# Kernel tuning notes

Measured on AMD Instinct MI355X. Metric: run time of the kernel, lower is better.

## Reference

```python
import jax, jax.numpy as jnp
import numpy as np


def setup_inputs() -> dict:
    key = jax.random.key(0)
    k1, k2, k3 = jax.random.split(key, 3)
    N, E, D_IN, D_OUT = 100000, 1600000, 64, 64
    x = jax.random.normal(k1, (N, D_IN), dtype=jnp.float32)
    edge_index = jax.random.randint(k2, (2, E), 0, N, dtype=jnp.int64)
    # Glorot-style init for the GCN weight, zero bias (PyG defaults)
    W = jax.random.normal(k3, (D_IN, D_OUT), dtype=jnp.float32) * (1.0 / np.sqrt(D_IN))
    b = jnp.zeros((D_OUT,), dtype=jnp.float32)
    return {"x": x, "edge_index": edge_index, "W": W, "b": b}


def reference(x, edge_index, W, b):
    # GCNConv (PyG semantics, add_self_loops=True, normalize=True) followed by
    # Dropout (eval mode -> identity) and ReLU.
    N = x.shape[0]
    # Linear transform first (small GEMM)
    xw = x @ W  # [N, D_OUT]
    # Add self-loops
    loops = jnp.arange(N, dtype=edge_index.dtype)
    row = jnp.concatenate([edge_index[0], loops])  # source nodes
    col = jnp.concatenate([edge_index[1], loops])  # destination nodes
    # Symmetric degree normalization: deg over destination index (PyG gcn_norm)
    ones = jnp.ones(col.shape[0], dtype=xw.dtype)
    deg = jax.ops.segment_sum(ones, col, num_segments=N)
    deg_inv_sqrt = jnp.where(deg > 0, jax.lax.rsqrt(deg), 0.0)
    norm = deg_inv_sqrt[row] * deg_inv_sqrt[col]  # [E+N]
    # Gather source features, scale, scatter-add to destinations
    msgs = norm[:, None] * xw[row]  # [E+N, D_OUT]
    out = jax.ops.segment_sum(msgs, col, num_segments=N)
    out = out + b
    # dropout in eval mode is identity
    return jax.nn.relu(out)
```

## Files before the change

kernel.cpp:

```cpp
#include <hip/hip_runtime.h>
#include <hip/hip_fp16.h>


#define D 64
#define BW 256
#define CAPB 4800
#define CAPL (CAPB + 3 * BW)
#define EPT 16
#define PART_T 512
#define EPB (PART_T * EPT)
#define NBMAX 512

typedef __attribute__((ext_vector_type(8))) short bf16x8;
typedef __attribute__((ext_vector_type(4))) float f32x4;

__device__ __forceinline__ unsigned short f2bf(float f) {
    unsigned u = __float_as_uint(f);
    u += 0x7FFFu + ((u >> 16) & 1u);
    return (unsigned short)(u >> 16);
}

__global__ __launch_bounds__(512)
void k_cnt(const int* __restrict__ col, int* __restrict__ cnts,
           unsigned short* __restrict__ WT, const float* __restrict__ W,
           unsigned short* __restrict__ xw_h, int E, int NBUCK, int N) {
    __shared__ int lh[NBMAX];
    int tid = threadIdx.x;
    for (int i = tid; i < NBUCK; i += 512) lh[i] = 0;
    __syncthreads();
    int e0 = blockIdx.x * EPB + tid;
#pragma unroll
    for (int i = 0; i < EPT; ++i) {
        int e = e0 + i * 512;
        if (e < E)
            atomicAdd(&lh[__builtin_nontemporal_load(col + e) >> 8], 1);
    }
    __syncthreads();
    size_t cb = (size_t)blockIdx.x * NBUCK;
    for (int j = tid; j < NBUCK; j += 512) cnts[cb + j] = lh[j];
    if (blockIdx.x == 0) {
        for (int i = tid; i < 4096; i += 512) {
            int n = i >> 6, k = i & 63;
            WT[i] = f2bf(W[k * 64 + n]);
        }
        if (tid < 32) ((unsigned*)xw_h)[(size_t)N * 32 + tid] = 0u;
    }
}

__global__ __launch_bounds__(256)
void k_scan(const int* __restrict__ cnts, int* __restrict__ bases,
            int* __restrict__ bsz, int NB1, int NBUCK) {
    __shared__ int wsum[4];
    int b = blockIdx.x, t = threadIdx.x, lane = t & 63, wv = t >> 6;
    int v = (t < NB1) ? cnts[(size_t)t * NBUCK + b] : 0;
    int inc = v;
#pragma unroll
    for (int o = 1; o < 64; o <<= 1) {
        int u = __shfl_up(inc, o);
        if (lane >= o) inc += u;
    }
    if (lane == 63) wsum[wv] = inc;
    __syncthreads();
    int woff = 0;
#pragma unroll
    for (int w = 0; w < 4; ++w) woff += (w < wv) ? wsum[w] : 0;
    if (t < NB1) bases[(size_t)t * NBUCK + b] = woff + inc - v;
    if (t == 255) bsz[b] = woff + inc;
}

__global__ __launch_bounds__(512, 4)
void k_part(const int* __restrict__ row, const int* __restrict__ col,
            const int* __restrict__ bases, int* __restrict__ dense,
            int E, int NBUCK) {
    __shared__ int lh[NBMAX];
    __shared__ int lst[NBMAX + 1];
    __shared__ int bas[NBMAX];
    __shared__ int wsc[8];
    __shared__ int srtv[EPB];
    int tid = threadIdx.x;
    size_t bb = (size_t)blockIdx.x * NBUCK;
    for (int i = tid; i < NBUCK; i += 512) {
        lh[i] = 0;
        bas[i] = bases[bb + i];
    }
    __syncthreads();
    int e0 = blockIdx.x * EPB + tid;
    int rr[EPT], cc[EPT], pp[EPT];
#pragma unroll
    for (int i = 0; i < EPT; ++i) {
        int e = e0 + i * 512;
        if (e < E) {
            cc[i] = __builtin_nontemporal_load(col + e);
            rr[i] = __builtin_nontemporal_load(row + e);
            pp[i] = atomicAdd(&lh[cc[i] >> 8], 1);
        } else {
            cc[i] = -1;
        }
    }
    __syncthreads();
    int lane = tid & 63, wv = tid >> 6;
    int v = (tid < NBUCK) ? lh[tid] : 0;
    int inc = v;
#pragma unroll
    for (int o = 1; o < 64; o <<= 1) {
        int u = __shfl_up(inc, o);
        if (lane >= o) inc += u;
    }
    if (lane == 63) wsc[wv] = inc;
    __syncthreads();
    int woff = 0;
#pragma unroll
    for (int w = 0; w < 8; ++w) woff += (w < wv) ? wsc[w] : 0;
    if (tid < NBUCK) lst[tid] = woff + inc - v;
    int tot = min(EPB, E - blockIdx.x * EPB);
    if (tid == 0) lst[NBUCK] = tot;
    __syncthreads();
#pragma unroll
    for (int i = 0; i < EPT; ++i) {
        if (cc[i] >= 0)
            srtv[lst[cc[i] >> 8] + pp[i]] = (rr[i] << 8) | (cc[i] & 255);
    }
    __syncthreads();
    for (int p = tid; p < tot; p += 512) {
        int lo = 0, hi = NBUCK;
        while (hi - lo > 1) {
            int mid = (lo + hi) >> 1;
            if (lst[mid] <= p) lo = mid; else hi = mid;
        }
        int gpos = bas[lo] + (p - lst[lo]);
        if (gpos < CAPB) dense[(size_t)lo * CAPB + gpos] = srtv[p];
    }
}

__global__ __launch_bounds__(256, 4)
void k_gemm(const float* __restrict__ x, const unsigned short* __restrict__ WT,
            const int* __restrict__ dense, const int* __restrict__ bsz,
            unsigned char* __restrict__ deg8, unsigned short* __restrict__ xw_h,
            int N, int NT) {
    __shared__ int lh[BW];
    int tid = threadIdx.x, b = blockIdx.x;
    lh[tid] = 0;
    __syncthreads();
    int tot = min(bsz[b], CAPB);
    const int* dn = dense + (size_t)b * CAPB;
    for (int i = tid; i < tot; i += 256)
        atomicAdd(&lh[__builtin_nontemporal_load(dn + i) & 255], 1);
    __syncthreads();
    {
        int node = b * BW + tid;
        if (node < N) deg8[node] = (unsigned char)min(lh[tid], 255);
    }
    int lane = tid & 63, wv = tid >> 6;
    int m = lane & 15, quad = lane >> 4;
    bf16x8 Bf[4][2];
#pragma unroll
    for (int t = 0; t < 4; ++t)
#pragma unroll
        for (int s = 0; s < 2; ++s)
            Bf[t][s] = *(const bf16x8*)(WT + (t * 16 + m) * 64 + s * 32 + quad * 8);
#pragma unroll
    for (int s = 0; s < 4; ++s) {
        int mt = b * 16 + s * 4 + wv;
        if (mt >= NT) continue;
        int row0 = mt * 16;
        const float* xr = x + (size_t)(row0 + m) * 64 + quad * 8;
        f32x4 a0 = __builtin_nontemporal_load((const f32x4*)(xr));
        f32x4 a1 = __builtin_nontemporal_load((const f32x4*)(xr + 4));
        f32x4 a2 = __builtin_nontemporal_load((const f32x4*)(xr + 32));
        f32x4 a3 = __builtin_nontemporal_load((const f32x4*)(xr + 36));
        bf16x8 A0, A1;
        A0[0] = (short)f2bf(a0[0]); A0[1] = (short)f2bf(a0[1]);
        A0[2] = (short)f2bf(a0[2]); A0[3] = (short)f2bf(a0[3]);
        A0[4] = (short)f2bf(a1[0]); A0[5] = (short)f2bf(a1[1]);
        A0[6] = (short)f2bf(a1[2]); A0[7] = (short)f2bf(a1[3]);
        A1[0] = (short)f2bf(a2[0]); A1[1] = (short)f2bf(a2[1]);
        A1[2] = (short)f2bf(a2[2]); A1[3] = (short)f2bf(a2[3]);
        A1[4] = (short)f2bf(a3[0]); A1[5] = (short)f2bf(a3[1]);
        A1[6] = (short)f2bf(a3[2]); A1[7] = (short)f2bf(a3[3]);
        f32x4 acc[4];
#pragma unroll
        for (int t = 0; t < 4; ++t) {
            acc[t] = (f32x4){0.f, 0.f, 0.f, 0.f};
            acc[t] = __builtin_amdgcn_mfma_f32_16x16x32_bf16(Bf[t][0], A0, acc[t], 0, 0, 0);
            acc[t] = __builtin_amdgcn_mfma_f32_16x16x32_bf16(Bf[t][1], A1, acc[t], 0, 0, 0);
        }
        float dsc = rsqrtf((float)(lh[(row0 + m) & 255] + 1));
        unsigned short* op = xw_h + (size_t)(row0 + m) * 64 + quad * 4;
#pragma unroll
        for (int t = 0; t < 4; ++t) {
            __half2 h0, h1;
            h0.x = __float2half(acc[t][0] * dsc); h0.y = __float2half(acc[t][1] * dsc);
            h1.x = __float2half(acc[t][2] * dsc); h1.y = __float2half(acc[t][3] * dsc);
            uint2 u; u.x = *(unsigned*)&h0; u.y = *(unsigned*)&h1;
            *(uint2*)(op + t * 16) = u;
        }
    }
}

__global__ __launch_bounds__(512, 4)
void k_gather(const int* __restrict__ dense, const int* __restrict__ bsz,
              const unsigned char* __restrict__ deg8,
              const uint2* __restrict__ xwh, const float* __restrict__ bias,
              float* __restrict__ out, int N) {
    __shared__ int lh[BW], stt[BW], cur[BW];
    __shared__ int wsum[4];
    __shared__ __align__(16) int srtL[CAPL];
    int b = blockIdx.x, tid = threadIdx.x, lane = tid & 63;
    int v = 0, vp = 0, inc = 0;
    if (tid < BW) {
        int node = b * BW + tid;
        v = (node < N) ? (int)deg8[node] : 0;
        lh[tid] = v;
        vp = (v + 3) & ~3; inc = vp;
#pragma unroll
        for (int o = 1; o < 64; o <<= 1) {
            int u = __shfl_up(inc, o);
            if (lane >= o) inc += u;
        }
        if (lane == 63) wsum[tid >> 6] = inc;
    }
    __syncthreads();
    if (tid < BW) {
        int wv4 = tid >> 6, woff = 0;
#pragma unroll
        for (int w = 0; w < 4; ++w) woff += (w < wv4) ? wsum[w] : 0;
        int st = woff + inc - vp;
        stt[tid] = st;
        cur[tid] = st;
    }
    __syncthreads();
    int tot = min(bsz[b], CAPB);
    const int* dn = dense + (size_t)b * CAPB;
    for (int i = tid; i < tot; i += 512) {
        int val = __builtin_nontemporal_load(dn + i);
        int pos = atomicAdd(&cur[val & 255], 1);
        if (pos < CAPL) srtL[pos] = val >> 8;
    }
    __syncthreads();
    if (tid < BW) {
        int e = stt[tid] + v, ep = min(stt[tid] + vp, CAPL);
        for (; e < ep; ++e) srtL[e] = N;
    }
    __syncthreads();
    int l = lane & 15;
    int ng = lane >> 4;
    int wv = tid >> 6;
    const float4 bb = ((const float4*)bias)[l];
#define ADDV(h)                                                     \
    {                                                               \
        __half2 h0 = *(__half2*)&(h).x, h1 = *(__half2*)&(h).y;     \
        float2 f0 = __half22float2(h0), f1 = __half22float2(h1);    \
        acc.x += f0.x; acc.y += f0.y; acc.z += f1.x; acc.w += f1.y; \
    }
    for (int g = 0; g < 8; ++g) {
        int nn = wv * 32 + g * 4 + ng;
        int node = b * BW + nn;
        bool active = node < N;
        float4 acc = make_float4(0.f, 0.f, 0.f, 0.f);
        int k = 0, s0 = 0;
        if (active) {
            k = lh[nn]; s0 = stt[nn];
            uint2 hs = xwh[(size_t)node * 16 + l];
            ADDV(hs);
        }
        int kp = (k + 3) & ~3;
        if (s0 + kp > CAPL) kp = (CAPL > s0) ? ((CAPL - s0) & ~3) : 0;
        if (kp > 0) {
            int4 rv = *(const int4*)&srtL[s0];
            int j = 0;
            while (true) {
                uint2 va = xwh[(size_t)rv.x * 16 + l];
                uint2 vb = xwh[(size_t)rv.y * 16 + l];
                uint2 vc = xwh[(size_t)rv.z * 16 + l];
                uint2 vd = xwh[(size_t)rv.w * 16 + l];
                j += 4;
                bool more = j < kp;
                if (more) rv = *(const int4*)&srtL[s0 + j];
                ADDV(va); ADDV(vb); ADDV(vc); ADDV(vd);
                if (!more) break;
            }
        }
        if (active) {
            float dn2 = rsqrtf((float)(k + 1));
            f32x4 o;
            o[0] = fmaxf(fmaf(dn2, acc.x, bb.x), 0.f);
            o[1] = fmaxf(fmaf(dn2, acc.y, bb.y), 0.f);
            o[2] = fmaxf(fmaf(dn2, acc.z, bb.z), 0.f);
            o[3] = fmaxf(fmaf(dn2, acc.w, bb.w), 0.f);
            __builtin_nontemporal_store(o, (f32x4*)(out + ((size_t)node * 16 + l) * 4));
        }
    }
#undef ADDV
}

extern "C" void kernel_launch(void* const* d_in, const int* in_sizes, int n_in,
                              void* d_out, int out_size, void* d_ws, size_t ws_size,
                              hipStream_t stream) {
    const float* x    = (const float*)d_in[0];
    const int*   ei   = (const int*)d_in[1];
    const float* W    = (const float*)d_in[2];
    const float* bias = (const float*)d_in[3];
    float* out = (float*)d_out;

    const int N = in_sizes[0] / D;
    const int E = in_sizes[1] / 2;
    const int* row = ei;
    const int* col = ei + E;

    const int NBUCK = (N + BW - 1) / BW;
    const int NB1   = (E + EPB - 1) / EPB;
    const int NT    = (N + 15) / 16;

    char* ws = (char*)d_ws;
    size_t o = 0;
    unsigned short* xw_h = (unsigned short*)(ws + o);
    o += (size_t)(N + 1) * D * sizeof(unsigned short);
    int* dense = (int*)(ws + o); o += (size_t)NBUCK * CAPB * sizeof(int);
    int* cnts  = (int*)(ws + o); o += (size_t)NB1 * NBUCK * sizeof(int);
    int* bases = (int*)(ws + o); o += (size_t)NB1 * NBUCK * sizeof(int);
    int* bsz   = (int*)(ws + o); o += (size_t)NBUCK * sizeof(int);
    o = (o + 15) & ~(size_t)15;
    unsigned char* deg8 = (unsigned char*)(ws + o); o += (size_t)N;
    o = (o + 15) & ~(size_t)15;
    unsigned short* WT = (unsigned short*)(ws + o); o += 4096 * sizeof(unsigned short);

    k_cnt <<<NB1,   512, 0, stream>>>(col, cnts, WT, W, xw_h, E, NBUCK, N);
    k_scan<<<NBUCK, 256, 0, stream>>>(cnts, bases, bsz, NB1, NBUCK);
    k_part<<<NB1,   512, 0, stream>>>(row, col, bases, dense, E, NBUCK);
    k_gemm<<<NBUCK, 256, 0, stream>>>(x, WT, dense, bsz, deg8, xw_h, N, NT);
    k_gather<<<NBUCK, 512, 0, stream>>>(dense, bsz, deg8, (const uint2*)xw_h,
                                        bias, out, N);
}
```

Measured before the change: 172.5 us.

## Replace count/scan passes with atomic bucket reservation and persistent half-bucket gather

Drops the separate counting and scan kernels. Each partition block now reserves its slice of every destination bucket with a global atomicAdd on padded counters, which a memset clears first. The gather kernel becomes a persistent grid of 512 blocks that pull half-bucket work items from an atomic ticket, using a smaller LDS list for more occupancy and a software-pipelined neighbour load loop. This removes one full pass over the edges and a kernel launch. In exchange, edge order within a bucket becomes nondeterministic, the gather filters every bucket entry twice, and a shrunken per-half capacity could truncate high-degree halves.

```diff
diff --git a/kernel.cpp b/kernel.cpp
--- a/kernel.cpp
+++ b/kernel.cpp
@@ -5,11 +5,12 @@
 #define D 64
 #define BW 256
 #define CAPB 4800
-#define CAPL (CAPB + 3 * BW)
+#define CAPL 2944
 #define EPT 16
 #define PART_T 512
 #define EPB (PART_T * EPT)
 #define NBMAX 512
+#define GSTRIDE 16
 
 typedef __attribute__((ext_vector_type(8))) short bf16x8;
 typedef __attribute__((ext_vector_type(4))) float f32x4;
@@ -21,74 +22,24 @@
 }
 
 __global__ __launch_bounds__(512)
-void k_cnt(const int* __restrict__ col, int* __restrict__ cnts,
-           unsigned short* __restrict__ WT, const float* __restrict__ W,
-           unsigned short* __restrict__ xw_h, int E, int NBUCK, int N) {
-    __shared__ int lh[NBMAX];
-    int tid = threadIdx.x;
-    for (int i = tid; i < NBUCK; i += 512) lh[i] = 0;
-    __syncthreads();
-    int e0 = blockIdx.x * EPB + tid;
-#pragma unroll
-    for (int i = 0; i < EPT; ++i) {
-        int e = e0 + i * 512;
-        if (e < E)
-            atomicAdd(&lh[__builtin_nontemporal_load(col + e) >> 8], 1);
-    }
-    __syncthreads();
-    size_t cb = (size_t)blockIdx.x * NBUCK;
-    for (int j = tid; j < NBUCK; j += 512) cnts[cb + j] = lh[j];
-    if (blockIdx.x == 0) {
-        for (int i = tid; i < 4096; i += 512) {
-            int n = i >> 6, k = i & 63;
-            WT[i] = f2bf(W[k * 64 + n]);
-        }
-        if (tid < 32) ((unsigned*)xw_h)[(size_t)N * 32 + tid] = 0u;
-    }
-}
-
-__global__ __launch_bounds__(256)
-void k_scan(const int* __restrict__ cnts, int* __restrict__ bases,
-            int* __restrict__ bsz, int NB1, int NBUCK) {
-    __shared__ int wsum[4];
-    int b = blockIdx.x, t = threadIdx.x, lane = t & 63, wv = t >> 6;
-    int v = (t < NB1) ? cnts[(size_t)t * NBUCK + b] : 0;
-    int inc = v;
-#pragma unroll
-    for (int o = 1; o < 64; o <<= 1) {
-        int u = __shfl_up(inc, o);
-        if (lane >= o) inc += u;
-    }
-    if (lane == 63) wsum[wv] = inc;
-    __syncthreads();
-    int woff = 0;
-#pragma unroll
-    for (int w = 0; w < 4; ++w) woff += (w < wv) ? wsum[w] : 0;
-    if (t < NB1) bases[(size_t)t * NBUCK + b] = woff + inc - v;
-    if (t == 255) bsz[b] = woff + inc;
-}
-
-__global__ __launch_bounds__(512, 4)
 void k_part(const int* __restrict__ row, const int* __restrict__ col,
-            const int* __restrict__ bases, int* __restrict__ dense,
-            int E, int NBUCK) {
+            int* __restrict__ gcur, int* __restrict__ dense,
+            unsigned short* __restrict__ WT, const float* __restrict__ W,
+            unsigned short* __restrict__ xw_h,
+            int E, int NBUCK, int N) {
     __shared__ int lh[NBMAX];
     __shared__ int lst[NBMAX + 1];
     __shared__ int bas[NBMAX];
     __shared__ int wsc[8];
     __shared__ int srtv[EPB];
     int tid = threadIdx.x;
-    size_t bb = (size_t)blockIdx.x * NBUCK;
-    for (int i = tid; i < NBUCK; i += 512) {
-        lh[i] = 0;
-        bas[i] = bases[bb + i];
-    }
+    for (int i = tid; i < NBUCK; i += PART_T) lh[i] = 0;
     __syncthreads();
     int e0 = blockIdx.x * EPB + tid;
     int rr[EPT], cc[EPT], pp[EPT];
 #pragma unroll
     for (int i = 0; i < EPT; ++i) {
-        int e = e0 + i * 512;
+        int e = e0 + i * PART_T;
         if (e < E) {
             cc[i] = __builtin_nontemporal_load(col + e);
             rr[i] = __builtin_nontemporal_load(row + e);
@@ -98,6 +49,12 @@
         }
     }
     __syncthreads();
+    int rot = (int)((blockIdx.x * 97u) % (unsigned)NBUCK);
+    for (int j = tid; j < NBUCK; j += PART_T) {
+        int bu = j + rot; if (bu >= NBUCK) bu -= NBUCK;
+        int h = lh[bu];
+        if (h > 0) bas[bu] = atomicAdd(&gcur[bu * GSTRIDE], h);
+    }
     int lane = tid & 63, wv = tid >> 6;
     int v = (tid < NBUCK) ? lh[tid] : 0;
     int inc = v;
@@ -121,7 +78,7 @@
             srtv[lst[cc[i] >> 8] + pp[i]] = (rr[i] << 8) | (cc[i] & 255);
     }
     __syncthreads();
-    for (int p = tid; p < tot; p += 512) {
+    for (int p = tid; p < tot; p += PART_T) {
         int lo = 0, hi = NBUCK;
         while (hi - lo > 1) {
             int mid = (lo + hi) >> 1;
@@ -130,18 +87,25 @@
         int gpos = bas[lo] + (p - lst[lo]);
         if (gpos < CAPB) dense[(size_t)lo * CAPB + gpos] = srtv[p];
     }
+    if (blockIdx.x == 0) {
+        for (int i = tid; i < 4096; i += PART_T) {
+            int n = i >> 6, k = i & 63;
+            WT[i] = f2bf(W[k * 64 + n]);
+        }
+        if (tid < 32) ((unsigned*)xw_h)[(size_t)N * 32 + tid] = 0u;
+    }
 }
 
 __global__ __launch_bounds__(256, 4)
 void k_gemm(const float* __restrict__ x, const unsigned short* __restrict__ WT,
-            const int* __restrict__ dense, const int* __restrict__ bsz,
+            const int* __restrict__ dense, const int* __restrict__ gcur,
             unsigned char* __restrict__ deg8, unsigned short* __restrict__ xw_h,
             int N, int NT) {
     __shared__ int lh[BW];
     int tid = threadIdx.x, b = blockIdx.x;
     lh[tid] = 0;
     __syncthreads();
-    int tot = min(bsz[b], CAPB);
+    int tot = min(gcur[b * GSTRIDE], CAPB);
     const int* dn = dense + (size_t)b * CAPB;
     for (int i = tid; i < tot; i += 256)
         atomicAdd(&lh[__builtin_nontemporal_load(dn + i) & 255], 1);
@@ -197,51 +161,17 @@
     }
 }
 
-__global__ __launch_bounds__(512, 4)
-void k_gather(const int* __restrict__ dense, const int* __restrict__ bsz,
+__global__ __launch_bounds__(512, 2)
+void k_gather(const int* __restrict__ dense, const int* __restrict__ gcur,
               const unsigned char* __restrict__ deg8,
               const uint2* __restrict__ xwh, const float* __restrict__ bias,
-              float* __restrict__ out, int N) {
-    __shared__ int lh[BW], stt[BW], cur[BW];
-    __shared__ int wsum[4];
+              float* __restrict__ out, int* __restrict__ tick,
+              int N, int NBUCK) {
+    __shared__ int lh[128], stt[128], cur[128];
+    __shared__ int wsum[2];
+    __shared__ int sb;
     __shared__ __align__(16) int srtL[CAPL];
-    int b = blockIdx.x, tid = threadIdx.x, lane = tid & 63;
-    int v = 0, vp = 0, inc = 0;
-    if (tid < BW) {
-        int node = b * BW + tid;
-        v = (node < N) ? (int)deg8[node] : 0;
-        lh[tid] = v;
-        vp = (v + 3) & ~3; inc = vp;
-#pragma unroll
-        for (int o = 1; o < 64; o <<= 1) {
-            int u = __shfl_up(inc, o);
-            if (lane >= o) inc += u;
-        }
-        if (lane == 63) wsum[tid >> 6] = inc;
-    }
-    __syncthreads();
-    if (tid < BW) {
-        int wv4 = tid >> 6, woff = 0;
-#pragma unroll
-        for (int w = 0; w < 4; ++w) woff += (w < wv4) ? wsum[w] : 0;
-        int st = woff + inc - vp;
-        stt[tid] = st;
-        cur[tid] = st;
-    }
-    __syncthreads();
-    int tot = min(bsz[b], CAPB);
-    const int* dn = dense + (size_t)b * CAPB;
-    for (int i = tid; i < tot; i += 512) {
-        int val = __builtin_nontemporal_load(dn + i);
-        int pos = atomicAdd(&cur[val & 255], 1);
-        if (pos < CAPL) srtL[pos] = val >> 8;
-    }
-    __syncthreads();
-    if (tid < BW) {
-        int e = stt[tid] + v, ep = min(stt[tid] + vp, CAPL);
-        for (; e < ep; ++e) srtL[e] = N;
-    }
-    __syncthreads();
+    int tid = threadIdx.x, lane = tid & 63;
     int l = lane & 15;
     int ng = lane >> 4;
     int wv = tid >> 6;
@@ -252,43 +182,91 @@
         float2 f0 = __half22float2(h0), f1 = __half22float2(h1);    \
         acc.x += f0.x; acc.y += f0.y; acc.z += f1.x; acc.w += f1.y; \
     }
-    for (int g = 0; g < 8; ++g) {
-        int nn = wv * 32 + g * 4 + ng;
-        int node = b * BW + nn;
-        bool active = node < N;
-        float4 acc = make_float4(0.f, 0.f, 0.f, 0.f);
-        int k = 0, s0 = 0;
-        if (active) {
-            k = lh[nn]; s0 = stt[nn];
-            uint2 hs = xwh[(size_t)node * 16 + l];
-            ADDV(hs);
-        }
-        int kp = (k + 3) & ~3;
-        if (s0 + kp > CAPL) kp = (CAPL > s0) ? ((CAPL - s0) & ~3) : 0;
-        if (kp > 0) {
-            int4 rv = *(const int4*)&srtL[s0];
-            int j = 0;
-            while (true) {
+    while (true) {
+        if (tid == 0) sb = atomicAdd(tick, 1);
+        __syncthreads();
+        int t = sb;
+        if (t >= 2 * NBUCK) break;
+        int b = t >> 1, hf = t & 1;
+        int nb0 = b * BW + hf * 128;
+        int v = 0, vp = 0, inc = 0;
+        if (tid < 128) {
+            int node = nb0 + tid;
+            v = (node < N) ? (int)deg8[node] : 0;
+            lh[tid] = v;
+            vp = (v + 3) & ~3; inc = vp;
+#pragma unroll
+            for (int o = 1; o < 64; o <<= 1) {
+                int u = __shfl_up(inc, o);
+                if (lane >= o) inc += u;
+            }
+            if (lane == 63) wsum[tid >> 6] = inc;
+        }
+        __syncthreads();
+        if (tid < 128) {
+            int st = inc - vp + ((tid >> 6) ? wsum[0] : 0);
+            stt[tid] = st;
+            cur[tid] = st;
+        }
+        __syncthreads();
+        int tot = min(gcur[b * GSTRIDE], CAPB);
+        const int* dn = dense + (size_t)b * CAPB;
+        int hsel = hf << 7;
+        for (int i = tid; i < tot; i += 512) {
+            int val = __builtin_nontemporal_load(dn + i);
+            if ((val & 128) == hsel) {
+                int pos = atomicAdd(&cur[val & 127], 1);
+                if (pos < CAPL) srtL[pos] = val >> 8;
+            }
+        }
+        __syncthreads();
+        if (tid < 128) {
+            int e = stt[tid] + v, ep = min(stt[tid] + vp, CAPL);
+            for (; e < ep; ++e) srtL[e] = N;
+        }
+        __syncthreads();
+#pragma unroll
+        for (int g = 0; g < 4; ++g) {
+            int nn = g * 32 + wv * 4 + ng;
+            int node = nb0 + nn;
+            bool active = node < N;
+            float4 acc = make_float4(0.f, 0.f, 0.f, 0.f);
+            int k = 0, s0 = 0;
+            if (active) {
+                k = lh[nn]; s0 = stt[nn];
+                uint2 hs = xwh[(size_t)node * 16 + l];
+                ADDV(hs);
+            }
+            int kp = (k + 3) & ~3;
+            if (s0 + kp > CAPL) kp = (CAPL > s0) ? ((CAPL - s0) & ~3) : 0;
+            if (kp > 0) {
+                int4 rv = *(const int4*)&srtL[s0];
                 uint2 va = xwh[(size_t)rv.x * 16 + l];
                 uint2 vb = xwh[(size_t)rv.y * 16 + l];
                 uint2 vc = xwh[(size_t)rv.z * 16 + l];
                 uint2 vd = xwh[(size_t)rv.w * 16 + l];
-                j += 4;
-                bool more = j < kp;
-                if (more) rv = *(const int4*)&srtL[s0 + j];
+                for (int j = 4; j < kp; j += 4) {
+                    int4 r2 = *(const int4*)&srtL[s0 + j];
+                    uint2 wa = xwh[(size_t)r2.x * 16 + l];
+                    uint2 wb = xwh[(size_t)r2.y * 16 + l];
+                    uint2 wc = xwh[(size_t)r2.z * 16 + l];
+                    uint2 wd = xwh[(size_t)r2.w * 16 + l];
+                    ADDV(va); ADDV(vb); ADDV(vc); ADDV(vd);
+                    va = wa; vb = wb; vc = wc; vd = wd;
+                }
                 ADDV(va); ADDV(vb); ADDV(vc); ADDV(vd);
-                if (!more) break;
-            }
-        }
-        if (active) {
-            float dn2 = rsqrtf((float)(k + 1));
-            f32x4 o;
-            o[0] = fmaxf(fmaf(dn2, acc.x, bb.x), 0.f);
-            o[1] = fmaxf(fmaf(dn2, acc.y, bb.y), 0.f);
-            o[2] = fmaxf(fmaf(dn2, acc.z, bb.z), 0.f);
-            o[3] = fmaxf(fmaf(dn2, acc.w, bb.w), 0.f);
-            __builtin_nontemporal_store(o, (f32x4*)(out + ((size_t)node * 16 + l) * 4));
-        }
+            }
+            if (active) {
+                float dn2 = rsqrtf((float)(k + 1));
+                f32x4 o;
+                o[0] = fmaxf(fmaf(dn2, acc.x, bb.x), 0.f);
+                o[1] = fmaxf(fmaf(dn2, acc.y, bb.y), 0.f);
+                o[2] = fmaxf(fmaf(dn2, acc.z, bb.z), 0.f);
+                o[3] = fmaxf(fmaf(dn2, acc.w, bb.w), 0.f);
+                __builtin_nontemporal_store(o, (f32x4*)(out + ((size_t)node * 16 + l) * 4));
+            }
+        }
+        __syncthreads();
     }
 #undef ADDV
 }
@@ -316,18 +294,15 @@
     unsigned short* xw_h = (unsigned short*)(ws + o);
     o += (size_t)(N + 1) * D * sizeof(unsigned short);
     int* dense = (int*)(ws + o); o += (size_t)NBUCK * CAPB * sizeof(int);
-    int* cnts  = (int*)(ws + o); o += (size_t)NB1 * NBUCK * sizeof(int);
-    int* bases = (int*)(ws + o); o += (size_t)NB1 * NBUCK * sizeof(int);
-    int* bsz   = (int*)(ws + o); o += (size_t)NBUCK * sizeof(int);
-    o = (o + 15) & ~(size_t)15;
+    int* gcur  = (int*)(ws + o); o += (size_t)NBUCK * GSTRIDE * sizeof(int);
+    int* tick  = (int*)(ws + o); o += 16 * sizeof(int);
     unsigned char* deg8 = (unsigned char*)(ws + o); o += (size_t)N;
     o = (o + 15) & ~(size_t)15;
     unsigned short* WT = (unsigned short*)(ws + o); o += 4096 * sizeof(unsigned short);
 
-    k_cnt <<<NB1,   512, 0, stream>>>(col, cnts, WT, W, xw_h, E, NBUCK, N);
-    k_scan<<<NBUCK, 256, 0, stream>>>(cnts, bases, bsz, NB1, NBUCK);
-    k_part<<<NB1,   512, 0, stream>>>(row, col, bases, dense, E, NBUCK);
-    k_gemm<<<NBUCK, 256, 0, stream>>>(x, WT, dense, bsz, deg8, xw_h, N, NT);
-    k_gather<<<NBUCK, 512, 0, stream>>>(dense, bsz, deg8, (const uint2*)xw_h,
-                                        bias, out, N);
-}
+    hipMemsetAsync(gcur, 0, ((size_t)NBUCK * GSTRIDE + 16) * sizeof(int), stream);
+    k_part<<<NB1, PART_T, 0, stream>>>(row, col, gcur, dense, WT, W, xw_h, E, NBUCK, N);
+    k_gemm<<<NBUCK, 256, 0, stream>>>(x, WT, dense, gcur, deg8, xw_h, N, NT);
+    k_gather<<<512, 512, 0, stream>>>(dense, gcur, deg8, (const uint2*)xw_h,
+                                      bias, out, tick, N, NBUCK);
+}
```

Result: no change. 175.3 us (+1.6%).
